# Kernel optimization log

Measured on AMD Instinct MI355X. Metric: run time of the kernel, lower is better.

The kernel has to match this reference:

```python
import jax, jax.numpy as jnp
import numpy as np

B, T, D = 4, 1024, 1024
H, HD = 16, 64
DFF = 4096
EPS = 1e-5


def _ln(x, g, b):
    mu = jnp.mean(x, axis=-1, keepdims=True)
    var = jnp.var(x, axis=-1, keepdims=True)
    return (x - mu) * jax.lax.rsqrt(var + EPS) * g + b


def _attn(q_in, kv_in, wq, bq, wk, bk, wv, bv, wo, bo):
    # q_in: [B,Tq,D], kv_in: [B,Tk,D]
    Tq, Tk = q_in.shape[1], kv_in.shape[1]
    q = (q_in @ wq + bq).reshape(B, Tq, H, HD).transpose(0, 2, 1, 3)
    k = (kv_in @ wk + bk).reshape(B, Tk, H, HD).transpose(0, 2, 1, 3)
    v = (kv_in @ wv + bv).reshape(B, Tk, H, HD).transpose(0, 2, 1, 3)
    att = jnp.einsum('bhqd,bhkd->bhqk', q, k) * (1.0 / np.sqrt(HD))
    causal = jnp.tril(jnp.ones((Tq, Tk), dtype=bool))
    att = jnp.where(causal, att, -jnp.inf)
    att = jax.nn.softmax(att, axis=-1)
    y = jnp.einsum('bhqk,bhkd->bhqd', att, v)
    y = y.transpose(0, 2, 1, 3).reshape(B, Tq, H * HD)
    return y @ wo + bo


def setup_inputs() -> dict:
    key = jax.random.key(0)
    ks = jax.random.split(key, 20)
    g = lambda k, shp, scale: (jax.random.normal(k, shp, jnp.float32) * scale)
    s_d = 1.0 / np.sqrt(D)
    s_f = 1.0 / np.sqrt(DFF)
    inp = {
        'x_encoder': jax.random.normal(ks[0], (B, T, D), jnp.float32),
        'x': jax.random.normal(ks[1], (B, T, D), jnp.float32),
        'ln1_g': jnp.ones((D,), jnp.float32), 'ln1_b': jnp.zeros((D,), jnp.float32),
        'ln2_g': jnp.ones((D,), jnp.float32), 'ln2_b': jnp.zeros((D,), jnp.float32),
        'sa_wq': g(ks[2], (D, D), s_d), 'sa_bq': jnp.zeros((D,), jnp.float32),
        'sa_wk': g(ks[3], (D, D), s_d), 'sa_bk': jnp.zeros((D,), jnp.float32),
        'sa_wv': g(ks[4], (D, D), s_d), 'sa_bv': jnp.zeros((D,), jnp.float32),
        'sa_wo': g(ks[5], (D, D), s_d), 'sa_bo': jnp.zeros((D,), jnp.float32),
        'ca_wq': g(ks[6], (D, D), s_d), 'ca_bq': jnp.zeros((D,), jnp.float32),
        'ca_wk': g(ks[7], (D, D), s_d), 'ca_bk': jnp.zeros((D,), jnp.float32),
        'ca_wv': g(ks[8], (D, D), s_d), 'ca_bv': jnp.zeros((D,), jnp.float32),
        'ca_wo': g(ks[9], (D, D), s_d), 'ca_bo': jnp.zeros((D,), jnp.float32),
        'mlp_w1': g(ks[10], (D, DFF), s_d), 'mlp_b1': jnp.zeros((DFF,), jnp.float32),
        'mlp_w2': g(ks[11], (DFF, D), s_f), 'mlp_b2': jnp.zeros((D,), jnp.float32),
    }
    return inp


def reference(x_encoder, x, ln1_g, ln1_b, ln2_g, ln2_b,
              sa_wq, sa_bq, sa_wk, sa_bk, sa_wv, sa_bv, sa_wo, sa_bo,
              ca_wq, ca_bq, ca_wk, ca_bk, ca_wv, ca_bv, ca_wo, ca_bo,
              mlp_w1, mlp_b1, mlp_w2, mlp_b2):
    # x = x + SelfAttn(ln1(x))
    x = x + _attn(_ln(x, ln1_g, ln1_b), _ln(x, ln1_g, ln1_b),
                  sa_wq, sa_bq, sa_wk, sa_bk, sa_wv, sa_bv, sa_wo, sa_bo)
    # x = x + CrossAttn(x_encoder, ln1(x))  (note: ln1 reused, causal mask on dec x enc)
    x = x + _attn(_ln(x, ln1_g, ln1_b), x_encoder,
                  ca_wq, ca_bq, ca_wk, ca_bk, ca_wv, ca_bv, ca_wo, ca_bo)
    # MLP with exact GELU (torch nn.GELU default)
    h = _ln(x, ln2_g, ln2_b)
    h = jax.nn.gelu(h @ mlp_w1 + mlp_b1, approximate=False) @ mlp_w2 + mlp_b2
    return x + h
```

## Files before the change

kernel.cpp:

```cpp
#include <hip/hip_runtime.h>
#include <hip/hip_bf16.h>

typedef __bf16 bf16;
typedef __attribute__((ext_vector_type(4))) __bf16 bf16x4;
typedef __attribute__((ext_vector_type(8))) __bf16 bf16x8;
typedef __attribute__((ext_vector_type(4))) float f32x4;

#define MFMA16(a, b, c) __builtin_amdgcn_mfma_f32_16x16x32_bf16(a, b, c, 0, 0, 0)

#define LGKM_FENCE()                                      \
  do {                                                    \
    asm volatile("s_waitcnt lgkmcnt(0)" ::: "memory");    \
    __builtin_amdgcn_sched_barrier(0);                    \
  } while (0)

#define SCHED0() __builtin_amdgcn_sched_barrier(0)
#define SBAR() __builtin_amdgcn_s_barrier()
#define PRIO(x) __builtin_amdgcn_s_setprio(x)

typedef __attribute__((address_space(1))) void gvoid;
typedef __attribute__((address_space(3))) void lvoid;
__device__ __forceinline__ void gl16(const bf16* g, bf16* l) {
  __builtin_amdgcn_global_load_lds((gvoid*)g, (lvoid*)l, 16, 0, 0);
}


struct WPtrs { const float* p[8]; };

__global__ __launch_bounds__(256) void wtrans8_k(WPtrs wp, bf16* __restrict__ dst) {
  const float* w = wp.p[blockIdx.z];
  bf16* wt = dst + (size_t)blockIdx.z * 1024 * 1024;
  __shared__ float t[32][33];
  const int tx = threadIdx.x & 31, ty = threadIdx.x >> 5;
  const int nb = blockIdx.x * 32, kb = blockIdx.y * 32;
  for (int i = 0; i < 4; ++i)
    t[ty + i * 8][tx] = w[(size_t)(kb + ty + i * 8) * 1024 + nb + tx];
  __syncthreads();
  for (int i = 0; i < 4; ++i)
    wt[(size_t)(nb + ty + i * 8) * 1024 + kb + tx] = (bf16)t[tx][ty + i * 8];
}

__global__ __launch_bounds__(256) void wtrans_k(const float* __restrict__ w,
                                                bf16* __restrict__ wt,
                                                int K, int N) {
  __shared__ float t[32][33];
  const int tx = threadIdx.x & 31, ty = threadIdx.x >> 5;
  const int nb = blockIdx.x * 32, kb = blockIdx.y * 32;
  for (int i = 0; i < 4; ++i)
    t[ty + i * 8][tx] = w[(size_t)(kb + ty + i * 8) * N + nb + tx];
  __syncthreads();
  for (int i = 0; i < 4; ++i)
    wt[(size_t)(nb + ty + i * 8) * K + kb + tx] = (bf16)t[tx][ty + i * 8];
}

__global__ __launch_bounds__(256) void tobf_k(const float* __restrict__ in,
                                              bf16* __restrict__ out) {
  const int i = blockIdx.x * 256 + threadIdx.x;
  const float4 v = ((const float4*)in)[i];
  bf16* o = out + (size_t)i * 4;
  o[0] = (bf16)v.x; o[1] = (bf16)v.y; o[2] = (bf16)v.z; o[3] = (bf16)v.w;
}

struct B5 { const float* s[5]; };
__global__ __launch_bounds__(256) void bpack_k(B5 bp, float* __restrict__ bq3,
                                               float* __restrict__ bkv2) {
  const int i = blockIdx.x;
  float* d = (i < 3) ? bq3 + i * 1024 : bkv2 + (i - 3) * 1024;
  ((float4*)d)[threadIdx.x] = ((const float4*)bp.s[i])[threadIdx.x];
}

__global__ __launch_bounds__(512) void vtrans_k(const bf16* __restrict__ V0,
                                                const bf16* __restrict__ V1,
                                                bf16* __restrict__ T0,
                                                bf16* __restrict__ T1) {
  const bf16* Vp = blockIdx.z ? V1 : V0;
  bf16* Vt = blockIdx.z ? T1 : T0;
  __shared__ bf16 tl[64][72];
  const int tt = blockIdx.x, bh = blockIdx.y;
  const int b = bh >> 4, h = bh & 15;
  const int tid = threadIdx.x;
  const int row = tid >> 3, ck = tid & 7;
  *(bf16x8*)&tl[row][ck * 8] =
      *(const bf16x8*)&Vp[(size_t)(b * 1024 + tt * 64 + row) * 1024 + h * 64 + ck * 8];
  __syncthreads();
  const int hd = tid >> 3, tc = tid & 7;
  bf16 tmp[8];
#pragma unroll
  for (int e = 0; e < 8; ++e) tmp[e] = tl[tc * 8 + e][hd];
  *(bf16x8*)&Vt[(size_t)(bh * 64 + hd) * 1024 + tt * 64 + tc * 8] = *(bf16x8*)tmp;
}

template <typename TIN>
__global__ __launch_bounds__(256) void ln_k(const TIN* __restrict__ x,
                                            const float* __restrict__ g,
                                            const float* __restrict__ bta,
                                            bf16* __restrict__ out) {
  const int row = blockIdx.x, tid = threadIdx.x;
  float v0, v1, v2, v3;
  if constexpr (sizeof(TIN) == 4) {
    const float4 v = ((const float4*)((const float*)x + (size_t)row * 1024))[tid];
    v0 = v.x; v1 = v.y; v2 = v.z; v3 = v.w;
  } else {
    const bf16x4 v = *(const bf16x4*)((const bf16*)x + (size_t)row * 1024 + tid * 4);
    v0 = (float)v[0]; v1 = (float)v[1]; v2 = (float)v[2]; v3 = (float)v[3];
  }
  float s = v0 + v1 + v2 + v3;
  float sq = v0 * v0 + v1 * v1 + v2 * v2 + v3 * v3;
  for (int d = 1; d < 64; d <<= 1) { s += __shfl_xor(s, d); sq += __shfl_xor(sq, d); }
  __shared__ float rs[4], rq[4];
  const int w = tid >> 6, lane = tid & 63;
  if (lane == 0) { rs[w] = s; rq[w] = sq; }
  __syncthreads();
  s = rs[0] + rs[1] + rs[2] + rs[3];
  sq = rq[0] + rq[1] + rq[2] + rq[3];
  const float mean = s * (1.0f / 1024.0f);
  const float var = sq * (1.0f / 1024.0f) - mean * mean;
  const float rstd = rsqrtf(var + 1e-5f);
  const float4 gv = ((const float4*)g)[tid];
  const float4 bv = ((const float4*)bta)[tid];
  bf16* o = out + (size_t)row * 1024 + tid * 4;
  o[0] = (bf16)((v0 - mean) * rstd * gv.x + bv.x);
  o[1] = (bf16)((v1 - mean) * rstd * gv.y + bv.y);
  o[2] = (bf16)((v2 - mean) * rstd * gv.z + bv.z);
  o[3] = (bf16)((v3 - mean) * rstd * gv.w + bv.w);
}

template <int EPI>
__global__ __launch_bounds__(256) void gemm_k(const bf16* __restrict__ A,
                                              const bf16* __restrict__ Bt,
                                              const float* __restrict__ bias,
                                              void* __restrict__ o0,
                                              int K, int N) {
  __shared__ bf16 As[2][128 * 64];
  __shared__ bf16 Bs[2][128 * 64];
  const int tid = threadIdx.x;
  const int lane = tid & 63, w = tid >> 6;
  const int wr = w >> 1, wc = w & 1;
  const int l15 = lane & 15, l4 = lane >> 4;
  const int gx = gridDim.x;
  const int nwg = gx * gridDim.y;
  const int flat = blockIdx.x + blockIdx.y * gx;
  const int swz = (flat & 7) * (nwg >> 3) + (flat >> 3);
  const size_t bm = swz / gx, bn = swz % gx;
  const bf16* Ab = A + bm * 128 * (size_t)K;
  const bf16* Bb = Bt + bn * 128 * (size_t)K;

  const f32x4 zero4 = {0.f, 0.f, 0.f, 0.f};
  f32x4 acc[4][4];
  for (int m = 0; m < 4; ++m)
    for (int n = 0; n < 4; ++n) acc[m][n] = zero4;

  const int srow = lane >> 3;
  const int gck = ((lane & 7) ^ srow) * 8;
  auto stage = [&](int buf, int t) {
    const int kt = t * 64;
    for (int j = 0; j < 4; ++j) {
      const int row = w * 32 + j * 8 + srow;
      bf16* la = As[buf] + (w * 256 + j * 64 + lane) * 8;
      bf16* lb = Bs[buf] + (w * 256 + j * 64 + lane) * 8;
      gl16(Ab + (size_t)row * K + kt + gck, la);
      gl16(Bb + (size_t)row * K + kt + gck, lb);
    }
  };
  const int xr = l15 & 7;
  const int c0 = (l4 ^ xr) * 8, c1 = ((4 + l4) ^ xr) * 8;
  auto compute = [&](int buf) {
    bf16x8 af[4][2], bfr[4][2];
    for (int m = 0; m < 4; ++m) {
      const int ro = (wr * 64 + m * 16 + l15) * 64;
      af[m][0] = *(const bf16x8*)&As[buf][ro + c0];
      af[m][1] = *(const bf16x8*)&As[buf][ro + c1];
    }
    for (int n = 0; n < 4; ++n) {
      const int ro = (wc * 64 + n * 16 + l15) * 64;
      bfr[n][0] = *(const bf16x8*)&Bs[buf][ro + c0];
      bfr[n][1] = *(const bf16x8*)&Bs[buf][ro + c1];
    }
    PRIO(1);
    for (int m = 0; m < 4; ++m)
      for (int n = 0; n < 4; ++n) {
        acc[m][n] = MFMA16(af[m][0], bfr[n][0], acc[m][n]);
        acc[m][n] = MFMA16(af[m][1], bfr[n][1], acc[m][n]);
      }
    PRIO(0);
  };

  const int nt = K >> 6;
  stage(0, 0);
  stage(1, 1);
  int cur = 0;
  for (int t = 0; t < nt - 2; ++t) {
    asm volatile("s_waitcnt vmcnt(8)" ::: "memory");
    SBAR(); SCHED0();
    compute(cur);
    SCHED0(); SBAR(); SCHED0();
    stage(cur, t + 2);
    cur ^= 1;
  }
  asm volatile("s_waitcnt vmcnt(8)" ::: "memory");
  SBAR(); SCHED0();
  compute(cur);
  cur ^= 1;
  asm volatile("s_waitcnt vmcnt(0)" ::: "memory");
  SBAR(); SCHED0();
  compute(cur);

  for (int m = 0; m < 4; ++m) {
    const int row0 = (int)bm * 128 + wr * 64 + m * 16 + l4 * 4;
    for (int n = 0; n < 4; ++n) {
      const int col = (int)bn * 128 + wc * 64 + n * 16 + l15;
      const float bv = bias[col];
      for (int r = 0; r < 4; ++r) {
        const int row = row0 + r;
        const float v = acc[m][n][r] + bv;
        const float gl = 0.5f * v * (1.0f + erff(v * 0.70710678118f));
        ((bf16*)o0)[(size_t)row * N + col] = (bf16)gl;
      }
    }
  }
}

__global__ __launch_bounds__(256) void gemmqkv_k(const bf16* __restrict__ Aln,
                                                 const bf16* __restrict__ Axe,
                                                 const bf16* __restrict__ wtq,
                                                 const bf16* __restrict__ wtkv,
                                                 const float* __restrict__ bq3,
                                                 const float* __restrict__ bkv2,
                                                 bf16* __restrict__ Qb,
                                                 bf16* __restrict__ Kb1,
                                                 bf16* __restrict__ Vp1,
                                                 bf16* __restrict__ Kb2,
                                                 bf16* __restrict__ Vp2) {
  const int K = 1024;
  __shared__ bf16 As[2][128 * 64];
  __shared__ bf16 Bs[2][128 * 64];
  const int tid = threadIdx.x;
  const int lane = tid & 63, w = tid >> 6;
  const int wr = w >> 1, wc = w & 1;
  const int l15 = lane & 15, l4 = lane >> 4;
  const int gx = 40;
  const int nwg = 40 * 32;
  const int flat = blockIdx.x + blockIdx.y * gx;
  const int swz = (flat & 7) * (nwg >> 3) + (flat >> 3);
  const size_t bm = swz / gx, bn = swz % gx;
  const bool qkv = bn < 24;
  const bf16* Ab = (qkv ? Aln : Axe) + bm * 128 * (size_t)K;
  const bf16* Bb = qkv ? (wtq + bn * 128 * (size_t)K)
                       : (wtkv + (bn - 24) * 128 * (size_t)K);

  const f32x4 zero4 = {0.f, 0.f, 0.f, 0.f};
  f32x4 acc[4][4];
  for (int m = 0; m < 4; ++m)
    for (int n = 0; n < 4; ++n) acc[m][n] = zero4;

  const int srow = lane >> 3;
  const int gck = ((lane & 7) ^ srow) * 8;
  auto stage = [&](int buf, int t) {
    const int kt = t * 64;
    for (int j = 0; j < 4; ++j) {
      const int row = w * 32 + j * 8 + srow;
      bf16* la = As[buf] + (w * 256 + j * 64 + lane) * 8;
      bf16* lb = Bs[buf] + (w * 256 + j * 64 + lane) * 8;
      gl16(Ab + (size_t)row * K + kt + gck, la);
      gl16(Bb + (size_t)row * K + kt + gck, lb);
    }
  };
  const int xr = l15 & 7;
  const int c0 = (l4 ^ xr) * 8, c1 = ((4 + l4) ^ xr) * 8;
  auto compute = [&](int buf) {
    bf16x8 af[4][2], bfr[4][2];
    for (int m = 0; m < 4; ++m) {
      const int ro = (wr * 64 + m * 16 + l15) * 64;
      af[m][0] = *(const bf16x8*)&As[buf][ro + c0];
      af[m][1] = *(const bf16x8*)&As[buf][ro + c1];
    }
    for (int n = 0; n < 4; ++n) {
      const int ro = (wc * 64 + n * 16 + l15) * 64;
      bfr[n][0] = *(const bf16x8*)&Bs[buf][ro + c0];
      bfr[n][1] = *(const bf16x8*)&Bs[buf][ro + c1];
    }
    PRIO(1);
    for (int m = 0; m < 4; ++m)
      for (int n = 0; n < 4; ++n) {
        acc[m][n] = MFMA16(af[m][0], bfr[n][0], acc[m][n]);
        acc[m][n] = MFMA16(af[m][1], bfr[n][1], acc[m][n]);
      }
    PRIO(0);
  };

  const int nt = K >> 6;
  stage(0, 0);
  stage(1, 1);
  int cur = 0;
  for (int t = 0; t < nt - 2; ++t) {
    asm volatile("s_waitcnt vmcnt(8)" ::: "memory");
    SBAR(); SCHED0();
    compute(cur);
    SCHED0(); SBAR(); SCHED0();
    stage(cur, t + 2);
    cur ^= 1;
  }
  asm volatile("s_waitcnt vmcnt(8)" ::: "memory");
  SBAR(); SCHED0();
  compute(cur);
  cur ^= 1;
  asm volatile("s_waitcnt vmcnt(0)" ::: "memory");
  SBAR(); SCHED0();
  compute(cur);

  for (int m = 0; m < 4; ++m) {
    const int row0 = (int)bm * 128 + wr * 64 + m * 16 + l4 * 4;
    for (int n = 0; n < 4; ++n) {
      const int coln = (qkv ? (int)bn : (int)bn - 24) * 128 + wc * 64 + n * 16 + l15;
      const float bv = qkv ? bq3[coln] : bkv2[coln];
      const int which = coln >> 10, c = coln & 1023;
      bf16* op = qkv ? (which == 0 ? Qb : (which == 1 ? Kb1 : Vp1))
                     : (which == 0 ? Kb2 : Vp2);
      for (int r = 0; r < 4; ++r) {
        const int row = row0 + r;
        op[(size_t)row * 1024 + c] = (bf16)(acc[m][n][r] + bv);
      }
    }
  }
}

template <int EPI>
__global__ __launch_bounds__(256) void gemm64_k(const bf16* __restrict__ A,
                                                const bf16* __restrict__ Bt,
                                                const float* __restrict__ bias,
                                                const void* __restrict__ res,
                                                void* __restrict__ o0,
                                                int K, int N) {
  __shared__ bf16 As[2][128 * 64];
  __shared__ bf16 Bs[2][64 * 64];
  const int tid = threadIdx.x;
  const int lane = tid & 63, w = tid >> 6;
  const int l15 = lane & 15, l4 = lane >> 4;
  const int gx = gridDim.x;
  const int nwg = gx * gridDim.y;
  const int flat = blockIdx.x + blockIdx.y * gx;
  const int swz = (flat & 7) * (nwg >> 3) + (flat >> 3);
  const size_t bm = swz / gx, bn = swz % gx;
  const bf16* Ab = A + bm * 128 * (size_t)K;
  const bf16* Bb = Bt + bn * 64 * (size_t)K;

  const f32x4 zero4 = {0.f, 0.f, 0.f, 0.f};
  f32x4 acc[2][4];
  for (int m = 0; m < 2; ++m)
    for (int n = 0; n < 4; ++n) acc[m][n] = zero4;

  const int srow = lane >> 3;
  const int gck = ((lane & 7) ^ srow) * 8;
  auto stage = [&](int buf, int t) {
    const int kt = t * 64;
    for (int j = 0; j < 4; ++j) {
      const int row = w * 32 + j * 8 + srow;
      gl16(Ab + (size_t)row * K + kt + gck, As[buf] + (w * 256 + j * 64 + lane) * 8);
    }
    for (int j = 0; j < 2; ++j) {
      const int row = w * 16 + j * 8 + srow;
      gl16(Bb + (size_t)row * K + kt + gck, Bs[buf] + (w * 128 + j * 64 + lane) * 8);
    }
  };
  const int xr = l15 & 7;
  const int c0 = (l4 ^ xr) * 8, c1 = ((4 + l4) ^ xr) * 8;
  auto compute = [&](int buf) {
    bf16x8 af[2][2], bfr[4][2];
    for (int m = 0; m < 2; ++m) {
      const int ro = (w * 32 + m * 16 + l15) * 64;
      af[m][0] = *(const bf16x8*)&As[buf][ro + c0];
      af[m][1] = *(const bf16x8*)&As[buf][ro + c1];
    }
    for (int n = 0; n < 4; ++n) {
      const int ro = (n * 16 + l15) * 64;
      bfr[n][0] = *(const bf16x8*)&Bs[buf][ro + c0];
      bfr[n][1] = *(const bf16x8*)&Bs[buf][ro + c1];
    }
    PRIO(1);
    for (int m = 0; m < 2; ++m)
      for (int n = 0; n < 4; ++n) {
        acc[m][n] = MFMA16(af[m][0], bfr[n][0], acc[m][n]);
        acc[m][n] = MFMA16(af[m][1], bfr[n][1], acc[m][n]);
      }
    PRIO(0);
  };

  const int nt = K >> 6;
  stage(0, 0);
  stage(1, 1);
  int cur = 0;
  for (int t = 0; t < nt - 2; ++t) {
    asm volatile("s_waitcnt vmcnt(6)" ::: "memory");
    SBAR(); SCHED0();
    compute(cur);
    SCHED0(); SBAR(); SCHED0();
    stage(cur, t + 2);
    cur ^= 1;
  }
  asm volatile("s_waitcnt vmcnt(6)" ::: "memory");
  SBAR(); SCHED0();
  compute(cur);
  cur ^= 1;
  asm volatile("s_waitcnt vmcnt(0)" ::: "memory");
  SBAR(); SCHED0();
  compute(cur);

  for (int m = 0; m < 2; ++m) {
    const int row0 = (int)bm * 128 + w * 32 + m * 16 + l4 * 4;
    for (int n = 0; n < 4; ++n) {
      const int col = (int)bn * 64 + n * 16 + l15;
      const float bv = bias[col];
      for (int r = 0; r < 4; ++r) {
        const int row = row0 + r;
        const size_t idx = (size_t)row * N + col;
        float v = acc[m][n][r] + bv;
        if constexpr (EPI == 0) {
          ((bf16*)o0)[idx] = (bf16)v;
        } else if constexpr (EPI == 2) {
          v += ((const float*)res)[idx];
          ((bf16*)o0)[idx] = (bf16)v;
        } else if constexpr (EPI == 4) {
          v += (float)((const bf16*)res)[idx];
          ((bf16*)o0)[idx] = (bf16)v;
        } else {
          v += (float)((const bf16*)res)[idx];
          ((float*)o0)[idx] = v;
        }
      }
    }
  }
}

__global__ __launch_bounds__(512) void attn_k(const bf16* __restrict__ Q,
                                              const bf16* __restrict__ Kb,
                                              const bf16* __restrict__ Vt,
                                              bf16* __restrict__ O) {
  __shared__ bf16 Ks[2][64 * 64];
  __shared__ bf16 Vs[2][64 * 64];
  __shared__ bf16 Plds[8][16][72];
  const int bx = blockIdx.x, bh = blockIdx.y;
  const int b = bh >> 4, h = bh & 15;
  const int tid = threadIdx.x, lane = tid & 63, w = tid >> 6;
  const int myqt = (w < 4) ? bx : (15 - bx);
  const int qbase = myqt * 64 + (w & 3) * 16;
  const int l15 = lane & 15, l4 = lane >> 4;
  const int nt = 16 - bx;

  const bf16* Qp = Q + (size_t)(b * 1024 + qbase + l15) * 1024 + h * 64 + l4 * 8;
  bf16x8 qf0 = *(const bf16x8*)Qp;
  bf16x8 qf1 = *(const bf16x8*)(Qp + 32);
  for (int i = 0; i < 8; ++i) {
    qf0[i] = (bf16)((float)qf0[i] * 0.125f);
    qf1[i] = (bf16)((float)qf1[i] * 0.125f);
  }
  bf16x8 onesf;
  for (int i = 0; i < 8; ++i) onesf[i] = (bf16)1.0f;

  const f32x4 zero4 = {0.f, 0.f, 0.f, 0.f};
  f32x4 o[4], ol;
  float mrow[4];
  for (int d = 0; d < 4; ++d) o[d] = zero4;
  ol = zero4;
  for (int r = 0; r < 4; ++r) mrow[r] = -1e30f;

  const int qrow0 = qbase + l4 * 4;

  const int srow = tid >> 3;
  const int cg = (tid & 7) ^ (srow & 7);
  const bf16* Kg = Kb + (size_t)(b * 1024 + srow) * 1024 + h * 64 + cg * 8;
  const bf16* Vg = Vt + (size_t)(bh * 64 + srow) * 1024 + cg * 8;
  auto stage = [&](int buf, int t) {
    gl16(Kg + (size_t)t * 64 * 1024, Ks[buf] + tid * 8);
    gl16(Vg + t * 64, Vs[buf] + tid * 8);
  };

  const int xr = l15 & 7;
  const int fc0 = (l4 ^ xr) * 8, fc1 = ((4 + l4) ^ xr) * 8;

  auto compute = [&](int buf, int kt) {
    const int kbase = kt * 64;
    f32x4 s[4];
    for (int n = 0; n < 4; ++n) s[n] = zero4;
    PRIO(1);
    for (int n = 0; n < 4; ++n) {
      const int ro = (n * 16 + l15) * 64;
      const bf16x8 kf0 = *(const bf16x8*)&Ks[buf][ro + fc0];
      const bf16x8 kf1 = *(const bf16x8*)&Ks[buf][ro + fc1];
      s[n] = MFMA16(qf0, kf0, s[n]);
      s[n] = MFMA16(qf1, kf1, s[n]);
    }
    PRIO(0);
    if (kt == myqt) {
      for (int n = 0; n < 4; ++n) {
        const int kc = kbase + n * 16 + l15;
        for (int r = 0; r < 4; ++r)
          if (kc > qrow0 + r) s[n][r] = -1e30f;
      }
    }
    float mx[4];
    for (int r = 0; r < 4; ++r)
      mx[r] = fmaxf(fmaxf(s[0][r], s[1][r]), fmaxf(s[2][r], s[3][r]));
    for (int d0 = 1; d0 < 16; d0 <<= 1)
      for (int r = 0; r < 4; ++r) mx[r] = fmaxf(mx[r], __shfl_xor(mx[r], d0));
    float alpha[4];
    for (int r = 0; r < 4; ++r) {
      const float mnew = fmaxf(mrow[r], mx[r]);
      alpha[r] = __expf(mrow[r] - mnew);
      mrow[r] = mnew;
    }
    for (int n = 0; n < 4; ++n)
      for (int r = 0; r < 4; ++r) s[n][r] = __expf(s[n][r] - mrow[r]);
    for (int d = 0; d < 4; ++d)
      for (int r = 0; r < 4; ++r) o[d][r] *= alpha[r];
    for (int r = 0; r < 4; ++r) ol[r] *= alpha[r];

    LGKM_FENCE();
    for (int r = 0; r < 4; ++r)
      for (int n = 0; n < 4; ++n)
        Plds[w][l4 * 4 + r][n * 16 + l15] = (bf16)s[n][r];
    LGKM_FENCE();
    const bf16x8 pf0 = *(const bf16x8*)&Plds[w][l15][l4 * 8];
    const bf16x8 pf1 = *(const bf16x8*)&Plds[w][l15][32 + l4 * 8];

    PRIO(1);
    for (int d = 0; d < 4; ++d) {
      const int ro = (d * 16 + l15) * 64;
      const bf16x8 vf0 = *(const bf16x8*)&Vs[buf][ro + fc0];
      const bf16x8 vf1 = *(const bf16x8*)&Vs[buf][ro + fc1];
      o[d] = MFMA16(pf0, vf0, o[d]);
      o[d] = MFMA16(pf1, vf1, o[d]);
    }
    ol = MFMA16(pf0, onesf, ol);
    ol = MFMA16(pf1, onesf, ol);
    PRIO(0);
  };

  stage(0, 0);
  stage(1, 1);
  int cur = 0;
  for (int t = 0; t < nt - 2; ++t) {
    asm volatile("s_waitcnt vmcnt(2)" ::: "memory");
    SBAR(); SCHED0();
    if (t <= myqt) compute(cur, t);
    SCHED0(); SBAR(); SCHED0();
    stage(cur, t + 2);
    cur ^= 1;
  }
  asm volatile("s_waitcnt vmcnt(2)" ::: "memory");
  SBAR(); SCHED0();
  if (nt - 2 <= myqt) compute(cur, nt - 2);
  cur ^= 1;
  asm volatile("s_waitcnt vmcnt(0)" ::: "memory");
  SBAR(); SCHED0();
  if (nt - 1 <= myqt) compute(cur, nt - 1);

  for (int r = 0; r < 4; ++r) {
    const float inv = 1.0f / ol[r];
    for (int d = 0; d < 4; ++d) {
      O[(size_t)(b * 1024 + qbase + l4 * 4 + r) * 1024 + h * 64 + d * 16 + l15] =
          (bf16)(o[d][r] * inv);
    }
  }
}

extern "C" void kernel_launch(void* const* d_in, const int* in_sizes, int n_in,
                              void* d_out, int out_size, void* d_ws, size_t ws_size,
                              hipStream_t stream) {
  const float* x_enc = (const float*)d_in[0];
  const float* x     = (const float*)d_in[1];
  const float* ln1_g = (const float*)d_in[2];
  const float* ln1_b = (const float*)d_in[3];
  const float* ln2_g = (const float*)d_in[4];
  const float* ln2_b = (const float*)d_in[5];
  const float* sa_wq = (const float*)d_in[6];  const float* sa_bq = (const float*)d_in[7];
  const float* sa_wk = (const float*)d_in[8];  const float* sa_bk = (const float*)d_in[9];
  const float* sa_wv = (const float*)d_in[10]; const float* sa_bv = (const float*)d_in[11];
  const float* sa_wo = (const float*)d_in[12]; const float* sa_bo = (const float*)d_in[13];
  const float* ca_wq = (const float*)d_in[14]; const float* ca_bq = (const float*)d_in[15];
  const float* ca_wk = (const float*)d_in[16]; const float* ca_bk = (const float*)d_in[17];
  const float* ca_wv = (const float*)d_in[18]; const float* ca_bv = (const float*)d_in[19];
  const float* ca_wo = (const float*)d_in[20]; const float* ca_bo = (const float*)d_in[21];
  const float* mlp_w1 = (const float*)d_in[22]; const float* mlp_b1 = (const float*)d_in[23];
  const float* mlp_w2 = (const float*)d_in[24]; const float* mlp_b2 = (const float*)d_in[25];

  char* ws = (char*)d_ws;
  size_t off = 0;
  auto take = [&](size_t bytes) { char* p = ws + off; off += (bytes + 255) & ~(size_t)255; return p; };

  bf16* wt8 = (bf16*)take((size_t)8 * 1024 * 1024 * 2);
  bf16* w1t   = (bf16*)take((size_t)4096 * 1024 * 2);
  bf16* w2t   = (bf16*)take((size_t)1024 * 4096 * 2);
  bf16* lnbuf = (bf16*)take((size_t)4096 * 1024 * 2);
  bf16* xe_bf = (bf16*)take((size_t)4096 * 1024 * 2);
  bf16* Qb    = (bf16*)take((size_t)4096 * 1024 * 2);
  bf16* Kb1   = (bf16*)take((size_t)4096 * 1024 * 2);
  bf16* Vp1   = (bf16*)take((size_t)4096 * 1024 * 2);
  bf16* Vt1   = (bf16*)take((size_t)4096 * 1024 * 2);
  bf16* Kb2   = (bf16*)take((size_t)4096 * 1024 * 2);
  bf16* Vp2   = (bf16*)take((size_t)4096 * 1024 * 2);
  bf16* Vt2   = (bf16*)take((size_t)4096 * 1024 * 2);
  bf16* AOb   = (bf16*)take((size_t)4096 * 1024 * 2);
  bf16* x1    = (bf16*)take((size_t)4096 * 1024 * 2);
  bf16* x2    = (bf16*)take((size_t)4096 * 1024 * 2);
  bf16* Hb    = (bf16*)take((size_t)4096 * 4096 * 2);
  float* bq3  = (float*)take((size_t)3072 * 4);
  float* bkv2 = (float*)take((size_t)2048 * 4);

  bf16* wt[8];
  for (int i = 0; i < 8; ++i) wt[i] = wt8 + (size_t)i * 1024 * 1024;

  const dim3 blk(256);
  WPtrs wp = {{sa_wq, sa_wk, sa_wv, sa_wo, ca_wq, ca_wk, ca_wv, ca_wo}};
  wtrans8_k<<<dim3(32, 32, 8), blk, 0, stream>>>(wp, wt8);
  wtrans_k<<<dim3(128, 32), blk, 0, stream>>>(mlp_w1, w1t, 1024, 4096);
  wtrans_k<<<dim3(32, 128), blk, 0, stream>>>(mlp_w2, w2t, 4096, 1024);
  tobf_k<<<4096, blk, 0, stream>>>(x_enc, xe_bf);
  B5 bp = {{sa_bq, sa_bk, sa_bv, ca_bk, ca_bv}};
  bpack_k<<<5, blk, 0, stream>>>(bp, bq3, bkv2);

  ln_k<float><<<4096, blk, 0, stream>>>(x, ln1_g, ln1_b, lnbuf);
  gemmqkv_k<<<dim3(40, 32), blk, 0, stream>>>(lnbuf, xe_bf, wt[0], wt[5],
                                              bq3, bkv2, Qb, Kb1, Vp1, Kb2, Vp2);
  vtrans_k<<<dim3(16, 64, 2), dim3(512), 0, stream>>>(Vp1, Vp2, Vt1, Vt2);

  attn_k<<<dim3(8, 64), dim3(512), 0, stream>>>(Qb, Kb1, Vt1, AOb);
  gemm64_k<2><<<dim3(16, 32), blk, 0, stream>>>(AOb, wt[3], sa_bo, x, x1, 1024, 1024);

  ln_k<bf16><<<4096, blk, 0, stream>>>(x1, ln1_g, ln1_b, lnbuf);
  gemm64_k<0><<<dim3(16, 32), blk, 0, stream>>>(lnbuf, wt[4], ca_bq, nullptr, Qb, 1024, 1024);
  attn_k<<<dim3(8, 64), dim3(512), 0, stream>>>(Qb, Kb2, Vt2, AOb);
  gemm64_k<4><<<dim3(16, 32), blk, 0, stream>>>(AOb, wt[7], ca_bo, x1, x2, 1024, 1024);

  ln_k<bf16><<<4096, blk, 0, stream>>>(x2, ln2_g, ln2_b, lnbuf);
  gemm_k<3><<<dim3(32, 32), blk, 0, stream>>>(lnbuf, w1t, mlp_b1, Hb, 1024, 4096);
  gemm64_k<5><<<dim3(16, 32), blk, 0, stream>>>(Hb, w2t, mlp_b2, x2,
                                                (float*)d_out, 4096, 1024);

  (void)in_sizes; (void)n_in; (void)out_size; (void)ws_size;
}
```

Before: 342.5 us.

## Replace double-buffered LDS pipeline with single-buffer load-sync-compute loop in GEMMs

Both the generic GEMM and the fused QKV GEMM drop the two-stage LDS ring with explicit vmcnt waits and prefetch two tiles ahead. They now use a single LDS buffer per operand, loading each K tile, synchronizing, computing, and synchronizing again. This halves shared memory per block, which could allow more resident blocks, but it serializes global-load latency with MFMA work. Correctness relies on __syncthreads waiting for the async global-to-LDS loads.

```diff
diff --git a/kernel.cpp b/kernel.cpp
--- a/kernel.cpp
+++ b/kernel.cpp
@@ -131,8 +131,8 @@
                                               const float* __restrict__ bias,
                                               void* __restrict__ o0,
                                               int K, int N) {
-  __shared__ bf16 As[2][128 * 64];
-  __shared__ bf16 Bs[2][128 * 64];
+  __shared__ bf16 As[128 * 64];
+  __shared__ bf16 Bs[128 * 64];
   const int tid = threadIdx.x;
   const int lane = tid & 63, w = tid >> 6;
   const int wr = w >> 1, wc = w & 1;
@@ -152,29 +152,30 @@
 
   const int srow = lane >> 3;
   const int gck = ((lane & 7) ^ srow) * 8;
-  auto stage = [&](int buf, int t) {
+  const int xr = l15 & 7;
+  const int c0 = (l4 ^ xr) * 8, c1 = ((4 + l4) ^ xr) * 8;
+
+  const int nt = K >> 6;
+  for (int t = 0; t < nt; ++t) {
     const int kt = t * 64;
     for (int j = 0; j < 4; ++j) {
       const int row = w * 32 + j * 8 + srow;
-      bf16* la = As[buf] + (w * 256 + j * 64 + lane) * 8;
-      bf16* lb = Bs[buf] + (w * 256 + j * 64 + lane) * 8;
+      bf16* la = As + (w * 256 + j * 64 + lane) * 8;
+      bf16* lb = Bs + (w * 256 + j * 64 + lane) * 8;
       gl16(Ab + (size_t)row * K + kt + gck, la);
       gl16(Bb + (size_t)row * K + kt + gck, lb);
     }
-  };
-  const int xr = l15 & 7;
-  const int c0 = (l4 ^ xr) * 8, c1 = ((4 + l4) ^ xr) * 8;
-  auto compute = [&](int buf) {
+    __syncthreads();
     bf16x8 af[4][2], bfr[4][2];
     for (int m = 0; m < 4; ++m) {
       const int ro = (wr * 64 + m * 16 + l15) * 64;
-      af[m][0] = *(const bf16x8*)&As[buf][ro + c0];
-      af[m][1] = *(const bf16x8*)&As[buf][ro + c1];
+      af[m][0] = *(const bf16x8*)&As[ro + c0];
+      af[m][1] = *(const bf16x8*)&As[ro + c1];
     }
     for (int n = 0; n < 4; ++n) {
       const int ro = (wc * 64 + n * 16 + l15) * 64;
-      bfr[n][0] = *(const bf16x8*)&Bs[buf][ro + c0];
-      bfr[n][1] = *(const bf16x8*)&Bs[buf][ro + c1];
+      bfr[n][0] = *(const bf16x8*)&Bs[ro + c0];
+      bfr[n][1] = *(const bf16x8*)&Bs[ro + c1];
     }
     PRIO(1);
     for (int m = 0; m < 4; ++m)
@@ -183,27 +184,8 @@
         acc[m][n] = MFMA16(af[m][1], bfr[n][1], acc[m][n]);
       }
     PRIO(0);
-  };
-
-  const int nt = K >> 6;
-  stage(0, 0);
-  stage(1, 1);
-  int cur = 0;
-  for (int t = 0; t < nt - 2; ++t) {
-    asm volatile("s_waitcnt vmcnt(8)" ::: "memory");
-    SBAR(); SCHED0();
-    compute(cur);
-    SCHED0(); SBAR(); SCHED0();
-    stage(cur, t + 2);
-    cur ^= 1;
-  }
-  asm volatile("s_waitcnt vmcnt(8)" ::: "memory");
-  SBAR(); SCHED0();
-  compute(cur);
-  cur ^= 1;
-  asm volatile("s_waitcnt vmcnt(0)" ::: "memory");
-  SBAR(); SCHED0();
-  compute(cur);
+    __syncthreads();
+  }
 
   for (int m = 0; m < 4; ++m) {
     const int row0 = (int)bm * 128 + wr * 64 + m * 16 + l4 * 4;
@@ -232,8 +214,8 @@
                                                  bf16* __restrict__ Kb2,
                                                  bf16* __restrict__ Vp2) {
   const int K = 1024;
-  __shared__ bf16 As[2][128 * 64];
-  __shared__ bf16 Bs[2][128 * 64];
+  __shared__ bf16 As[128 * 64];
+  __shared__ bf16 Bs[128 * 64];
   const int tid = threadIdx.x;
   const int lane = tid & 63, w = tid >> 6;
   const int wr = w >> 1, wc = w & 1;
@@ -255,29 +237,30 @@
 
   const int srow = lane >> 3;
   const int gck = ((lane & 7) ^ srow) * 8;
-  auto stage = [&](int buf, int t) {
+  const int xr = l15 & 7;
+  const int c0 = (l4 ^ xr) * 8, c1 = ((4 + l4) ^ xr) * 8;
+
+  const int nt = K >> 6;
+  for (int t = 0; t < nt; ++t) {
     const int kt = t * 64;
     for (int j = 0; j < 4; ++j) {
       const int row = w * 32 + j * 8 + srow;
-      bf16* la = As[buf] + (w * 256 + j * 64 + lane) * 8;
-      bf16* lb = Bs[buf] + (w * 256 + j * 64 + lane) * 8;
+      bf16* la = As + (w * 256 + j * 64 + lane) * 8;
+      bf16* lb = Bs + (w * 256 + j * 64 + lane) * 8;
       gl16(Ab + (size_t)row * K + kt + gck, la);
       gl16(Bb + (size_t)row * K + kt + gck, lb);
     }
-  };
-  const int xr = l15 & 7;
-  const int c0 = (l4 ^ xr) * 8, c1 = ((4 + l4) ^ xr) * 8;
-  auto compute = [&](int buf) {
+    __syncthreads();
     bf16x8 af[4][2], bfr[4][2];
     for (int m = 0; m < 4; ++m) {
       const int ro = (wr * 64 + m * 16 + l15) * 64;
-      af[m][0] = *(const bf16x8*)&As[buf][ro + c0];
-      af[m][1] = *(const bf16x8*)&As[buf][ro + c1];
+      af[m][0] = *(const bf16x8*)&As[ro + c0];
+      af[m][1] = *(const bf16x8*)&As[ro + c1];
     }
     for (int n = 0; n < 4; ++n) {
       const int ro = (wc * 64 + n * 16 + l15) * 64;
-      bfr[n][0] = *(const bf16x8*)&Bs[buf][ro + c0];
-      bfr[n][1] = *(const bf16x8*)&Bs[buf][ro + c1];
+      bfr[n][0] = *(const bf16x8*)&Bs[ro + c0];
+      bfr[n][1] = *(const bf16x8*)&Bs[ro + c1];
     }
     PRIO(1);
     for (int m = 0; m < 4; ++m)
@@ -286,27 +269,8 @@
         acc[m][n] = MFMA16(af[m][1], bfr[n][1], acc[m][n]);
       }
     PRIO(0);
-  };
-
-  const int nt = K >> 6;
-  stage(0, 0);
-  stage(1, 1);
-  int cur = 0;
-  for (int t = 0; t < nt - 2; ++t) {
-    asm volatile("s_waitcnt vmcnt(8)" ::: "memory");
-    SBAR(); SCHED0();
-    compute(cur);
-    SCHED0(); SBAR(); SCHED0();
-    stage(cur, t + 2);
-    cur ^= 1;
-  }
-  asm volatile("s_waitcnt vmcnt(8)" ::: "memory");
-  SBAR(); SCHED0();
-  compute(cur);
-  cur ^= 1;
-  asm volatile("s_waitcnt vmcnt(0)" ::: "memory");
-  SBAR(); SCHED0();
-  compute(cur);
+    __syncthreads();
+  }
 
   for (int m = 0; m < 4; ++m) {
     const int row0 = (int)bm * 128 + wr * 64 + m * 16 + l4 * 4;
```

New measurement: 349.0 us. No clear change (+1.9%).
